# Optimization experiments

Measured on AMD Instinct MI355X. Metric: run time of the kernel, lower is better.

Reference implementation:

```python
import jax, jax.numpy as jnp
import numpy as np


def conv1x1(x, w, b):
    # x: [B,C,H,W], w: [O,C], b: [O]  (1x1 conv == per-pixel matmul)
    return jnp.einsum('oc,bchw->bohw', w, x) + b[None, :, None, None]


def setup_inputs() -> dict:
    key = jax.random.key(0)
    ks = jax.random.split(key, 8)
    B, C, H, W = 8, 256, 64, 64
    heads, points = 8, 4
    x = jax.random.normal(ks[0], (B, C, H, W), dtype=jnp.float32)
    # small offset weights so sampling grids stay mostly in-range (original inits these to 0)
    w_off = jax.random.normal(ks[1], (heads * points * 2, C), dtype=jnp.float32) * 0.01
    b_off = jax.random.normal(ks[2], (heads * points * 2,), dtype=jnp.float32) * 0.05
    w_attn = jax.random.normal(ks[3], (heads * points, C), dtype=jnp.float32) * 0.02
    b_attn = jnp.full((heads * points,), np.log(1.0 / points), dtype=jnp.float32)
    w_val = jax.random.normal(ks[4], (C, C), dtype=jnp.float32) * (1.0 / np.sqrt(C))
    b_val = jnp.zeros((C,), dtype=jnp.float32)
    w_out = jax.random.normal(ks[5], (C, C), dtype=jnp.float32) * (1.0 / np.sqrt(C))
    b_out = jnp.zeros((C,), dtype=jnp.float32)
    return {"x": x, "w_off": w_off, "b_off": b_off, "w_attn": w_attn, "b_attn": b_attn,
            "w_val": w_val, "b_val": b_val, "w_out": w_out, "b_out": b_out,
            "num_heads": heads, "num_points": points}


def _grid_sample_one(v, g):
    # v: [Cph,H,W] value image; g: [P,H,W,2] sampling grid in [-1,1] (x,y), align_corners=True,
    # bilinear, zero padding. Returns [Cph,P,H,W].
    Cph, H, W = v.shape
    ix = (g[..., 0] + 1.0) * 0.5 * (W - 1)  # [P,H,W]
    iy = (g[..., 1] + 1.0) * 0.5 * (H - 1)
    x0 = jnp.floor(ix); y0 = jnp.floor(iy)
    x1 = x0 + 1.0;      y1 = y0 + 1.0
    wx1 = ix - x0; wx0 = 1.0 - wx1
    wy1 = iy - y0; wy0 = 1.0 - wy1

    def corner(yc, xc, w):
        valid = (xc >= 0) & (xc <= W - 1) & (yc >= 0) & (yc <= H - 1)
        yi = jnp.clip(yc, 0, H - 1).astype(jnp.int32)
        xi = jnp.clip(xc, 0, W - 1).astype(jnp.int32)
        vv = v[:, yi, xi]  # [Cph,P,H,W]
        return vv * (w * valid.astype(w.dtype))[None]

    return (corner(y0, x0, wy0 * wx0) + corner(y0, x1, wy0 * wx1)
            + corner(y1, x0, wy1 * wx0) + corner(y1, x1, wy1 * wx1))


def deformable_attention(x, w_off, b_off, w_attn, b_attn, w_val, b_val, w_out, b_out,
                         num_heads, num_points):
    B, C, H, W = x.shape
    hd, P = num_heads, num_points
    cph = C // hd

    value = conv1x1(x, w_val, b_val)                       # [B,C,H,W]
    offsets = conv1x1(x, w_off, b_off)                     # [B,hd*P*2,H,W]
    attn = conv1x1(x, w_attn, b_attn).reshape(B, hd, P, H, W)
    attn = jax.nn.softmax(attn, axis=2)                    # softmax over points

    gy = jnp.linspace(-1.0, 1.0, H, dtype=x.dtype)
    gx = jnp.linspace(-1.0, 1.0, W, dtype=x.dtype)
    base = jnp.stack(jnp.meshgrid(gx, gy, indexing='xy'), axis=-1)  # [H,W,2] (x,y)

    off = offsets.reshape(B, hd, P, 2, H, W).transpose(0, 1, 2, 4, 5, 3)  # [B,hd,P,H,W,2]
    grid = base[None, None, None] + off                                   # [B,hd,P,H,W,2]

    val = value.reshape(B * hd, cph, H, W)
    grid = grid.reshape(B * hd, P, H, W, 2)
    sampled = jax.vmap(_grid_sample_one)(val, grid)        # [B*hd,cph,P,H,W]
    sampled = sampled.reshape(B, hd, cph, P, H, W)

    weighted = (sampled * attn[:, :, None]).sum(axis=3)    # [B,hd,cph,H,W]
    weighted = weighted.reshape(B, C, H, W)
    return conv1x1(weighted, w_out, b_out) + x


def reference(x, w_off, b_off, w_attn, b_attn, w_val, b_val, w_out, b_out,
              num_heads, num_points):
    return deformable_attention(x, w_off, b_off, w_attn, b_attn, w_val, b_val,
                                w_out, b_out, num_heads, num_points)
```

## Files before the change

kernel.cpp:

```cpp
#include <hip/hip_runtime.h>
#include <cstddef>

#define HW 4096

typedef __attribute__((ext_vector_type(8))) short short8v;
typedef __attribute__((ext_vector_type(4))) float f32x4;

__device__ inline unsigned short f2bf(float f) {
    unsigned int u = __float_as_uint(f);
    u += 0x7FFFu + ((u >> 16) & 1u);
    return (unsigned short)(u >> 16);
}
__device__ inline float bf2f(unsigned short s) {
    return __uint_as_float(((unsigned int)s) << 16);
}

#define GLOAD_LDS16(gp, lp) __builtin_amdgcn_global_load_lds( \
    (const __attribute__((address_space(1))) unsigned int*)(gp), \
    (__attribute__((address_space(3))) unsigned int*)(lp), 16, 0, 0)

__device__ inline void stage_tile(const unsigned short* __restrict__ g,
                                  unsigned short* lds, int kc, int wid, int lane)
{
    const int r8   = lane >> 3;
    const int slot = (lane & 7) ^ r8;
    const unsigned short* src = g + (wid * 32 + r8) * 256 + kc + slot * 8;
#pragma unroll
    for (int i = 0; i < 4; ++i) {
        GLOAD_LDS16(src + i * 8 * 256, lds + (wid * 32 + i * 8) * 64);
    }
}

__device__ inline short8v read_frag(const unsigned short* lds, int row, int kbyte, int lane)
{
    const char* p = (const char*)lds + row * 128 + (kbyte ^ ((lane & 7) * 16));
    return *(const short8v*)p;
}

__global__ __launch_bounds__(256)
void prep_kernel(const float* __restrict__ w_off, const float* __restrict__ b_off,
                 const float* __restrict__ w_attn, const float* __restrict__ b_attn,
                 const float* __restrict__ w_val, const float* __restrict__ b_val,
                 const float* __restrict__ w_out,
                 unsigned short* __restrict__ wcat_bf, unsigned short* __restrict__ wauxlo,
                 unsigned short* __restrict__ wout_bf, float* __restrict__ bcat)
{
    int i = blockIdx.x * 256 + threadIdx.x;
    if (i < 384 * 256) {
        int n = i >> 8, k = i & 255;
        float v;
        if (n < 256)      v = w_val[n * 256 + k];
        else if (n < 320) v = w_off[(n - 256) * 256 + k];
        else if (n < 352) v = w_attn[(n - 320) * 256 + k];
        else              v = 0.0f;
        unsigned short hi = f2bf(v);
        wcat_bf[i] = hi;
        if (n >= 256) wauxlo[(n - 256) * 256 + k] = f2bf(v - bf2f(hi));
    }
    if (i < 256 * 256) wout_bf[i] = f2bf(w_out[i]);
    if (i < 512) {
        float v = 0.0f;
        if (i < 256)      v = b_val[i];
        else if (i < 320) v = b_off[i - 256];
        else if (i < 352) v = b_attn[i - 320];
        bcat[i] = v;
    }
}

__global__ __launch_bounds__(256)
void transpose_kernel(const float* __restrict__ x, unsigned short* __restrict__ xhi)
{
    __shared__ float t[64][65];
    const int bid = blockIdx.x;
    const int pt = bid & 63, ct = (bid >> 6) & 3, b = bid >> 8;
    const int tid = threadIdx.x;
    const int rr = tid >> 4, c4 = (tid & 15) * 4;

    const float* src = x + ((size_t)(b * 256 + ct * 64)) * HW + pt * 64;
#pragma unroll
    for (int j = 0; j < 4; ++j) {
        float4 v = *(const float4*)&src[(size_t)(j * 16 + rr) * HW + c4];
        t[j * 16 + rr][c4 + 0] = v.x; t[j * 16 + rr][c4 + 1] = v.y;
        t[j * 16 + rr][c4 + 2] = v.z; t[j * 16 + rr][c4 + 3] = v.w;
    }
    __syncthreads();

    const size_t obase = ((size_t)b * HW + pt * 64) * 256 + ct * 64;
#pragma unroll
    for (int j = 0; j < 4; ++j) {
        int p = j * 16 + rr;
        ushort4 hi = make_ushort4(f2bf(t[c4 + 0][p]), f2bf(t[c4 + 1][p]),
                                  f2bf(t[c4 + 2][p]), f2bf(t[c4 + 3][p]));
        *(ushort4*)&xhi[obase + (size_t)p * 256 + c4] = hi;
    }
}

__global__ __launch_bounds__(256)
void proj_kernel(const unsigned short* __restrict__ wcat_bf, const unsigned short* __restrict__ wauxlo,
                 const unsigned short* __restrict__ xhi, const float* __restrict__ bcat,
                 unsigned short* __restrict__ value_bf,
                 float* __restrict__ off_ws, float* __restrict__ attn_ws)
{
    __shared__ unsigned short lds[3 * 128 * 64];
    const int bid = blockIdx.x;
    const int mt = bid % 3;
    const int pt = (bid / 3) & 31;
    const int b  = bid / 96;
    const int tid = threadIdx.x, wid = tid >> 6, lane = tid & 63;
    const int wm = wid >> 1, wn = wid & 1;
    const int mloc = lane & 15, ksel = lane >> 4;

    const unsigned short* Bg = xhi + ((size_t)b * HW + pt * 128) * 256;

    f32x4 acc[4][4];
#pragma unroll
    for (int fm = 0; fm < 4; ++fm) {
        float4 bv = *(const float4*)&bcat[mt * 128 + wm * 64 + fm * 16 + ksel * 4];
#pragma unroll
        for (int fn = 0; fn < 4; ++fn) acc[fm][fn] = (f32x4){bv.x, bv.y, bv.z, bv.w};
    }

    if (mt < 2) {
        unsigned short* Al = lds;
        unsigned short* Bl = lds + 128 * 64;
        const unsigned short* Ag = wcat_bf + mt * 128 * 256;
#pragma unroll
        for (int kc = 0; kc < 4; ++kc) {
            if (kc) __syncthreads();
            stage_tile(Ag, Al, kc * 64, wid, lane);
            stage_tile(Bg, Bl, kc * 64, wid, lane);
            __syncthreads();
#pragma unroll
            for (int kk = 0; kk < 2; ++kk) {
                const int kb = kk * 64 + ksel * 16;
                short8v a[4], bb[4];
#pragma unroll
                for (int f = 0; f < 4; ++f) a[f]  = read_frag(Al, wm * 64 + f * 16 + mloc, kb, lane);
#pragma unroll
                for (int f = 0; f < 4; ++f) bb[f] = read_frag(Bl, wn * 64 + f * 16 + mloc, kb, lane);
#pragma unroll
                for (int fm = 0; fm < 4; ++fm)
#pragma unroll
                    for (int fn = 0; fn < 4; ++fn)
                        acc[fm][fn] = __builtin_amdgcn_mfma_f32_16x16x32_bf16(a[fm], bb[fn], acc[fm][fn], 0, 0, 0);
            }
        }
#pragma unroll
        for (int fm = 0; fm < 4; ++fm) {
            const int ch = mt * 128 + wm * 64 + fm * 16 + ksel * 4;
            const int head = ch >> 5, c32 = ch & 31;
#pragma unroll
            for (int fn = 0; fn < 4; ++fn) {
                const int p = pt * 128 + wn * 64 + fn * 16 + mloc;
                f32x4 v = acc[fm][fn];
                ushort4 st = make_ushort4(f2bf(v[0]), f2bf(v[1]), f2bf(v[2]), f2bf(v[3]));
                *(ushort4*)&value_bf[(((size_t)(b * 8 + head)) * HW + p) * 32 + c32] = st;
            }
        }
    } else {
        unsigned short* Ah  = lds;
        unsigned short* Alo = lds + 128 * 64;
        unsigned short* Bl  = lds + 2 * 128 * 64;
        const unsigned short* Ahg = wcat_bf + 256 * 256;
        const unsigned short* Alg = wauxlo;
#pragma unroll
        for (int kc = 0; kc < 4; ++kc) {
            if (kc) __syncthreads();
            stage_tile(Ahg, Ah, kc * 64, wid, lane);
            stage_tile(Alg, Alo, kc * 64, wid, lane);
            stage_tile(Bg, Bl, kc * 64, wid, lane);
            __syncthreads();
#pragma unroll
            for (int kk = 0; kk < 2; ++kk) {
                const int kb = kk * 64 + ksel * 16;
                short8v ah[4], al[4], bb[4];
#pragma unroll
                for (int f = 0; f < 4; ++f) {
                    ah[f] = read_frag(Ah,  wm * 64 + f * 16 + mloc, kb, lane);
                    al[f] = read_frag(Alo, wm * 64 + f * 16 + mloc, kb, lane);
                    bb[f] = read_frag(Bl,  wn * 64 + f * 16 + mloc, kb, lane);
                }
#pragma unroll
                for (int fm = 0; fm < 4; ++fm)
#pragma unroll
                    for (int fn = 0; fn < 4; ++fn) {
                        acc[fm][fn] = __builtin_amdgcn_mfma_f32_16x16x32_bf16(ah[fm], bb[fn], acc[fm][fn], 0, 0, 0);
                        acc[fm][fn] = __builtin_amdgcn_mfma_f32_16x16x32_bf16(al[fm], bb[fn], acc[fm][fn], 0, 0, 0);
                    }
            }
        }
#pragma unroll
        for (int fm = 0; fm < 4; ++fm) {
            const int chb = wm * 64 + fm * 16 + ksel * 4;
#pragma unroll
            for (int fn = 0; fn < 4; ++fn) {
                const int p = pt * 128 + wn * 64 + fn * 16 + mloc;
                f32x4 v = acc[fm][fn];
#pragma unroll
                for (int r = 0; r < 4; ++r) {
                    int ch = chb + r;
                    if (ch < 64)      off_ws[((size_t)(b * 64 + ch)) * HW + p] = v[r];
                    else if (ch < 96) attn_ws[((size_t)(b * 32 + (ch - 64))) * HW + p] = v[r];
                }
            }
        }
    }
}

__global__ __launch_bounds__(256)
void sample_kernel(const unsigned short* __restrict__ value_bf, const float* __restrict__ off_ws,
                   const float* __restrict__ attn_ws, unsigned short* __restrict__ wgt_t)
{
    const int bid    = blockIdx.x;
    const int ptile  = bid & 127;
    const int head   = (bid >> 7) & 7;
    const int b      = bid >> 10;
    const int tid    = threadIdx.x;
    const int c4     = tid & 7;
    const int posIdx = tid >> 3;
    const int p      = ptile * 32 + posIdx;
    const int h      = p >> 6;
    const int w      = p & 63;

    const float gx = w * (2.0f / 63.0f) - 1.0f;
    const float gy = h * (2.0f / 63.0f) - 1.0f;

    float l0 = attn_ws[(size_t)(b * 32 + head * 4 + 0) * HW + p];
    float l1 = attn_ws[(size_t)(b * 32 + head * 4 + 1) * HW + p];
    float l2 = attn_ws[(size_t)(b * 32 + head * 4 + 2) * HW + p];
    float l3 = attn_ws[(size_t)(b * 32 + head * 4 + 3) * HW + p];
    float m  = fmaxf(fmaxf(l0, l1), fmaxf(l2, l3));
    float e0 = __expf(l0 - m), e1 = __expf(l1 - m), e2 = __expf(l2 - m), e3 = __expf(l3 - m);
    float inv = 1.0f / (e0 + e1 + e2 + e3);
    float aw[4] = {e0 * inv, e1 * inv, e2 * inv, e3 * inv};

    float4 acc = make_float4(0.f, 0.f, 0.f, 0.f);
    const unsigned short* vb = value_bf + (size_t)(b * 8 + head) * HW * 32 + c4 * 4;

#pragma unroll
    for (int pt = 0; pt < 4; ++pt) {
        float ox = off_ws[(size_t)(b * 64 + (head * 4 + pt) * 2 + 0) * HW + p];
        float oy = off_ws[(size_t)(b * 64 + (head * 4 + pt) * 2 + 1) * HW + p];
        float ix = (gx + ox + 1.0f) * 31.5f;
        float iy = (gy + oy + 1.0f) * 31.5f;
        float x0f = floorf(ix), y0f = floorf(iy);
        float wx1 = ix - x0f, wx0 = 1.0f - wx1;
        float wy1 = iy - y0f, wy0 = 1.0f - wy1;
        int x0 = (int)x0f, y0 = (int)y0f;
        int x1 = x0 + 1,   y1 = y0 + 1;
        float a = aw[pt];
        float vx0 = (x0 >= 0 && x0 <= 63) ? 1.f : 0.f;
        float vx1 = (x1 >= 0 && x1 <= 63) ? 1.f : 0.f;
        float vy0 = (y0 >= 0 && y0 <= 63) ? 1.f : 0.f;
        float vy1 = (y1 >= 0 && y1 <= 63) ? 1.f : 0.f;
        float w00 = a * wy0 * wx0 * vy0 * vx0;
        float w01 = a * wy0 * wx1 * vy0 * vx1;
        float w10 = a * wy1 * wx0 * vy1 * vx0;
        float w11 = a * wy1 * wx1 * vy1 * vx1;
        int cx0 = min(max(x0, 0), 63), cx1 = min(max(x1, 0), 63);
        int cy0 = min(max(y0, 0), 63), cy1 = min(max(y1, 0), 63);
        ushort4 u00 = *(const ushort4*)&vb[(size_t)(cy0 * 64 + cx0) * 32];
        ushort4 u01 = *(const ushort4*)&vb[(size_t)(cy0 * 64 + cx1) * 32];
        ushort4 u10 = *(const ushort4*)&vb[(size_t)(cy1 * 64 + cx0) * 32];
        ushort4 u11 = *(const ushort4*)&vb[(size_t)(cy1 * 64 + cx1) * 32];
        acc.x += w00 * bf2f(u00.x) + w01 * bf2f(u01.x) + w10 * bf2f(u10.x) + w11 * bf2f(u11.x);
        acc.y += w00 * bf2f(u00.y) + w01 * bf2f(u01.y) + w10 * bf2f(u10.y) + w11 * bf2f(u11.y);
        acc.z += w00 * bf2f(u00.z) + w01 * bf2f(u01.z) + w10 * bf2f(u10.z) + w11 * bf2f(u11.z);
        acc.w += w00 * bf2f(u00.w) + w01 * bf2f(u01.w) + w10 * bf2f(u10.w) + w11 * bf2f(u11.w);
    }

    ushort4 st = make_ushort4(f2bf(acc.x), f2bf(acc.y), f2bf(acc.z), f2bf(acc.w));
    *(ushort4*)&wgt_t[((size_t)b * HW + p) * 256 + head * 32 + c4 * 4] = st;
}

__global__ __launch_bounds__(256)
void outproj_gemm(const unsigned short* __restrict__ wout_bf, const unsigned short* __restrict__ wgt_t,
                  const float* __restrict__ b_out, const float* __restrict__ x,
                  float* __restrict__ out)
{
    __shared__ unsigned short Al[128 * 64];
    __shared__ unsigned short Bl[128 * 64];
    const int bid = blockIdx.x;
    const int pt = bid & 31, mt = (bid >> 5) & 1, b = bid >> 6;
    const int tid = threadIdx.x, wid = tid >> 6, lane = tid & 63;
    const int wm = wid >> 1, wn = wid & 1;
    const int mloc = lane & 15, ksel = lane >> 4;

    const unsigned short* Ag = wout_bf + mt * 128 * 256;
    const unsigned short* Bg = wgt_t + ((size_t)b * HW + pt * 128) * 256;

    f32x4 acc[4][4];
#pragma unroll
    for (int fm = 0; fm < 4; ++fm)
#pragma unroll
        for (int fn = 0; fn < 4; ++fn) acc[fm][fn] = (f32x4){0.f, 0.f, 0.f, 0.f};

#pragma unroll
    for (int kc = 0; kc < 4; ++kc) {
        if (kc) __syncthreads();
        stage_tile(Ag, Al, kc * 64, wid, lane);
        stage_tile(Bg, Bl, kc * 64, wid, lane);
        __syncthreads();
#pragma unroll
        for (int kk = 0; kk < 2; ++kk) {
            const int kb = kk * 64 + ksel * 16;
            short8v a[4], bb[4];
#pragma unroll
            for (int f = 0; f < 4; ++f) a[f]  = read_frag(Al, wm * 64 + f * 16 + mloc, kb, lane);
#pragma unroll
            for (int f = 0; f < 4; ++f) bb[f] = read_frag(Bl, wn * 64 + f * 16 + mloc, kb, lane);
#pragma unroll
            for (int fm = 0; fm < 4; ++fm)
#pragma unroll
                for (int fn = 0; fn < 4; ++fn)
                    acc[fm][fn] = __builtin_amdgcn_mfma_f32_16x16x32_bf16(a[fm], bb[fn], acc[fm][fn], 0, 0, 0);
        }
    }

#pragma unroll
    for (int fm = 0; fm < 4; ++fm) {
        const int o = mt * 128 + wm * 64 + fm * 16 + ksel * 4;
        float4 bo = *(const float4*)&b_out[o];
#pragma unroll
        for (int fn = 0; fn < 4; ++fn) {
            const int p = pt * 128 + wn * 64 + fn * 16 + mloc;
            const size_t idx = ((size_t)(b * 256 + o)) * HW + p;
            f32x4 v = acc[fm][fn];
            out[idx + 0 * HW] = v[0] + bo.x + x[idx + 0 * HW];
            out[idx + 1 * HW] = v[1] + bo.y + x[idx + 1 * HW];
            out[idx + 2 * HW] = v[2] + bo.z + x[idx + 2 * HW];
            out[idx + 3 * HW] = v[3] + bo.w + x[idx + 3 * HW];
        }
    }
}

extern "C" void kernel_launch(void* const* d_in, const int* in_sizes, int n_in,
                              void* d_out, int out_size, void* d_ws, size_t ws_size,
                              hipStream_t stream)
{
    const float* x      = (const float*)d_in[0];
    const float* w_off  = (const float*)d_in[1];
    const float* b_off  = (const float*)d_in[2];
    const float* w_attn = (const float*)d_in[3];
    const float* b_attn = (const float*)d_in[4];
    const float* w_val  = (const float*)d_in[5];
    const float* b_val  = (const float*)d_in[6];
    const float* w_out  = (const float*)d_in[7];
    const float* b_out  = (const float*)d_in[8];
    float* out = (float*)d_out;

    char* ws = (char*)d_ws;
    unsigned short* wcat_bf = (unsigned short*)(ws + 0);
    unsigned short* wauxlo  = (unsigned short*)(ws + 196608);
    unsigned short* wout_bf = (unsigned short*)(ws + 262144);
    float*          bcat    = (float*)(ws + 393216);
    unsigned short* xhi     = (unsigned short*)(ws + 395264);
    unsigned short* val_bf  = (unsigned short*)(ws + 17172480);
    float*          off_ws  = (float*)(ws + 33949696);
    float*          attn_ws = (float*)(ws + 42338304);
    unsigned short* wgt_t   = (unsigned short*)(ws + 46532608);

    prep_kernel<<<384, 256, 0, stream>>>(w_off, b_off, w_attn, b_attn, w_val, b_val,
                                         w_out, wcat_bf, wauxlo, wout_bf, bcat);
    transpose_kernel<<<2048, 256, 0, stream>>>(x, xhi);
    proj_kernel<<<768, 256, 0, stream>>>(wcat_bf, wauxlo, xhi, bcat, val_bf, off_ws, attn_ws);
    sample_kernel<<<8192, 256, 0, stream>>>(val_bf, off_ws, attn_ws, wgt_t);
    outproj_gemm<<<512, 256, 0, stream>>>(wout_bf, wgt_t, b_out, x, out);
}
```

Measured before the change: 81.53 us.

## Stage full-K panels, transpose offset/attn layout, and LDS-stage outproj epilogue

The GEMM kernels now load the full K=256 panels for A and B into LDS in one pass using a row-XOR swizzle, replacing the four-chunk loop with its repeated barriers. The projection kernel reorders blocks so point tiles vary fastest, and runs the hi/lo aux weights as two sequential passes over the same B panel. Offset and attention logits are now stored pixel-major as float4, so the sample kernel reads them contiguously. The out-projection epilogue goes through LDS so the residual add and output store use coalesced float4 accesses. The larger LDS footprint (128 KB per block) limits occupancy to about one block per CU.

After: 80.73 us. No clear change (-1.0%).

```diff
diff --git a/kernel.cpp b/kernel.cpp
--- a/kernel.cpp
+++ b/kernel.cpp
@@ -19,22 +19,42 @@
     (const __attribute__((address_space(1))) unsigned int*)(gp), \
     (__attribute__((address_space(3))) unsigned int*)(lp), 16, 0, 0)
 
-__device__ inline void stage_tile(const unsigned short* __restrict__ g,
-                                  unsigned short* lds, int kc, int wid, int lane)
-{
-    const int r8   = lane >> 3;
-    const int slot = (lane & 7) ^ r8;
-    const unsigned short* src = g + (wid * 32 + r8) * 256 + kc + slot * 8;
-#pragma unroll
-    for (int i = 0; i < 4; ++i) {
-        GLOAD_LDS16(src + i * 8 * 256, lds + (wid * 32 + i * 8) * 64);
-    }
-}
-
-__device__ inline short8v read_frag(const unsigned short* lds, int row, int kbyte, int lane)
-{
-    const char* p = (const char*)lds + row * 128 + (kbyte ^ ((lane & 7) * 16));
+__device__ inline void stage_panel(const unsigned short* __restrict__ g,
+                                   unsigned short* lds, int wid, int lane)
+{
+    const int rsub = lane >> 5;
+    const int slot = lane & 31;
+#pragma unroll
+    for (int i = 0; i < 16; ++i) {
+        const int row = wid * 32 + i * 2 + rsub;
+        GLOAD_LDS16(g + row * 256 + ((slot ^ (row & 15)) << 3),
+                    lds + (wid * 32 + i * 2) * 256);
+    }
+}
+
+__device__ inline short8v read_frag256(const unsigned short* lds, int row, int kbyte)
+{
+    const char* p = (const char*)lds + row * 512 + (kbyte ^ ((row & 15) << 4));
     return *(const short8v*)p;
+}
+
+__device__ inline void compute_pass(const unsigned short* Al, const unsigned short* Bl,
+                                    int wm, int wn, int mloc, int ksel, f32x4 acc[4][4])
+{
+#pragma unroll
+    for (int kk = 0; kk < 8; ++kk) {
+        const int kb = kk * 64 + ksel * 16;
+        short8v a[4], bb[4];
+#pragma unroll
+        for (int f = 0; f < 4; ++f) a[f]  = read_frag256(Al, wm * 64 + f * 16 + mloc, kb);
+#pragma unroll
+        for (int f = 0; f < 4; ++f) bb[f] = read_frag256(Bl, wn * 64 + f * 16 + mloc, kb);
+#pragma unroll
+        for (int fm = 0; fm < 4; ++fm)
+#pragma unroll
+            for (int fn = 0; fn < 4; ++fn)
+                acc[fm][fn] = __builtin_amdgcn_mfma_f32_16x16x32_bf16(a[fm], bb[fn], acc[fm][fn], 0, 0, 0);
+    }
 }
 
 __global__ __launch_bounds__(256)
@@ -101,16 +121,19 @@
                  unsigned short* __restrict__ value_bf,
                  float* __restrict__ off_ws, float* __restrict__ attn_ws)
 {
-    __shared__ unsigned short lds[3 * 128 * 64];
+    __shared__ unsigned short smem[2 * 128 * 256];
+    unsigned short* Al = smem;
+    unsigned short* Bl = smem + 128 * 256;
+
     const int bid = blockIdx.x;
-    const int mt = bid % 3;
-    const int pt = (bid / 3) & 31;
+    const int pt = bid & 31;
+    const int mt = (bid >> 5) % 3;
     const int b  = bid / 96;
     const int tid = threadIdx.x, wid = tid >> 6, lane = tid & 63;
     const int wm = wid >> 1, wn = wid & 1;
     const int mloc = lane & 15, ksel = lane >> 4;
 
-    const unsigned short* Bg = xhi + ((size_t)b * HW + pt * 128) * 256;
+    stage_panel(xhi + ((size_t)b * HW + pt * 128) * 256, Bl, wid, lane);
 
     f32x4 acc[4][4];
 #pragma unroll
@@ -121,30 +144,10 @@
     }
 
     if (mt < 2) {
-        unsigned short* Al = lds;
-        unsigned short* Bl = lds + 128 * 64;
-        const unsigned short* Ag = wcat_bf + mt * 128 * 256;
-#pragma unroll
-        for (int kc = 0; kc < 4; ++kc) {
-            if (kc) __syncthreads();
-            stage_tile(Ag, Al, kc * 64, wid, lane);
-            stage_tile(Bg, Bl, kc * 64, wid, lane);
-            __syncthreads();
-#pragma unroll
-            for (int kk = 0; kk < 2; ++kk) {
-                const int kb = kk * 64 + ksel * 16;
-                short8v a[4], bb[4];
-#pragma unroll
-                for (int f = 0; f < 4; ++f) a[f]  = read_frag(Al, wm * 64 + f * 16 + mloc, kb, lane);
-#pragma unroll
-                for (int f = 0; f < 4; ++f) bb[f] = read_frag(Bl, wn * 64 + f * 16 + mloc, kb, lane);
-#pragma unroll
-                for (int fm = 0; fm < 4; ++fm)
-#pragma unroll
-                    for (int fn = 0; fn < 4; ++fn)
-                        acc[fm][fn] = __builtin_amdgcn_mfma_f32_16x16x32_bf16(a[fm], bb[fn], acc[fm][fn], 0, 0, 0);
-            }
-        }
+        stage_panel(wcat_bf + mt * 128 * 256, Al, wid, lane);
+        __syncthreads();
+        compute_pass(Al, Bl, wm, wn, mloc, ksel, acc);
+
 #pragma unroll
         for (int fm = 0; fm < 4; ++fm) {
             const int ch = mt * 128 + wm * 64 + fm * 16 + ksel * 4;
@@ -158,49 +161,27 @@
             }
         }
     } else {
-        unsigned short* Ah  = lds;
-        unsigned short* Alo = lds + 128 * 64;
-        unsigned short* Bl  = lds + 2 * 128 * 64;
-        const unsigned short* Ahg = wcat_bf + 256 * 256;
-        const unsigned short* Alg = wauxlo;
-#pragma unroll
-        for (int kc = 0; kc < 4; ++kc) {
-            if (kc) __syncthreads();
-            stage_tile(Ahg, Ah, kc * 64, wid, lane);
-            stage_tile(Alg, Alo, kc * 64, wid, lane);
-            stage_tile(Bg, Bl, kc * 64, wid, lane);
-            __syncthreads();
-#pragma unroll
-            for (int kk = 0; kk < 2; ++kk) {
-                const int kb = kk * 64 + ksel * 16;
-                short8v ah[4], al[4], bb[4];
-#pragma unroll
-                for (int f = 0; f < 4; ++f) {
-                    ah[f] = read_frag(Ah,  wm * 64 + f * 16 + mloc, kb, lane);
-                    al[f] = read_frag(Alo, wm * 64 + f * 16 + mloc, kb, lane);
-                    bb[f] = read_frag(Bl,  wn * 64 + f * 16 + mloc, kb, lane);
-                }
-#pragma unroll
-                for (int fm = 0; fm < 4; ++fm)
-#pragma unroll
-                    for (int fn = 0; fn < 4; ++fn) {
-                        acc[fm][fn] = __builtin_amdgcn_mfma_f32_16x16x32_bf16(ah[fm], bb[fn], acc[fm][fn], 0, 0, 0);
-                        acc[fm][fn] = __builtin_amdgcn_mfma_f32_16x16x32_bf16(al[fm], bb[fn], acc[fm][fn], 0, 0, 0);
-                    }
-            }
-        }
+        stage_panel(wcat_bf + 256 * 256, Al, wid, lane);
+        __syncthreads();
+        compute_pass(Al, Bl, wm, wn, mloc, ksel, acc);
+        __syncthreads();
+        stage_panel(wauxlo, Al, wid, lane);
+        __syncthreads();
+        compute_pass(Al, Bl, wm, wn, mloc, ksel, acc);
+
 #pragma unroll
         for (int fm = 0; fm < 4; ++fm) {
-            const int chb = wm * 64 + fm * 16 + ksel * 4;
+            const int ch0 = wm * 64 + fm * 16 + ksel * 4;
 #pragma unroll
             for (int fn = 0; fn < 4; ++fn) {
                 const int p = pt * 128 + wn * 64 + fn * 16 + mloc;
                 f32x4 v = acc[fm][fn];
-#pragma unroll
-                for (int r = 0; r < 4; ++r) {
-                    int ch = chb + r;
-                    if (ch < 64)      off_ws[((size_t)(b * 64 + ch)) * HW + p] = v[r];
-                    else if (ch < 96) attn_ws[((size_t)(b * 32 + (ch - 64))) * HW + p] = v[r];
+                if (ch0 < 64) {
+                    *(float4*)&off_ws[((size_t)b * HW + p) * 64 + ch0] =
+                        make_float4(v[0], v[1], v[2], v[3]);
+                } else if (ch0 < 96) {
+                    *(float4*)&attn_ws[((size_t)b * HW + p) * 32 + (ch0 - 64)] =
+                        make_float4(v[0], v[1], v[2], v[3]);
                 }
             }
         }
@@ -225,22 +206,20 @@
     const float gx = w * (2.0f / 63.0f) - 1.0f;
     const float gy = h * (2.0f / 63.0f) - 1.0f;
 
-    float l0 = attn_ws[(size_t)(b * 32 + head * 4 + 0) * HW + p];
-    float l1 = attn_ws[(size_t)(b * 32 + head * 4 + 1) * HW + p];
-    float l2 = attn_ws[(size_t)(b * 32 + head * 4 + 2) * HW + p];
-    float l3 = attn_ws[(size_t)(b * 32 + head * 4 + 3) * HW + p];
-    float m  = fmaxf(fmaxf(l0, l1), fmaxf(l2, l3));
-    float e0 = __expf(l0 - m), e1 = __expf(l1 - m), e2 = __expf(l2 - m), e3 = __expf(l3 - m);
+    float4 la = *(const float4*)&attn_ws[((size_t)b * HW + p) * 32 + head * 4];
+    float m  = fmaxf(fmaxf(la.x, la.y), fmaxf(la.z, la.w));
+    float e0 = __expf(la.x - m), e1 = __expf(la.y - m), e2 = __expf(la.z - m), e3 = __expf(la.w - m);
     float inv = 1.0f / (e0 + e1 + e2 + e3);
     float aw[4] = {e0 * inv, e1 * inv, e2 * inv, e3 * inv};
 
     float4 acc = make_float4(0.f, 0.f, 0.f, 0.f);
     const unsigned short* vb = value_bf + (size_t)(b * 8 + head) * HW * 32 + c4 * 4;
+    const float* offp = off_ws + ((size_t)b * HW + p) * 64 + head * 8;
 
 #pragma unroll
     for (int pt = 0; pt < 4; ++pt) {
-        float ox = off_ws[(size_t)(b * 64 + (head * 4 + pt) * 2 + 0) * HW + p];
-        float oy = off_ws[(size_t)(b * 64 + (head * 4 + pt) * 2 + 1) * HW + p];
+        float ox = offp[pt * 2 + 0];
+        float oy = offp[pt * 2 + 1];
         float ix = (gx + ox + 1.0f) * 31.5f;
         float iy = (gy + oy + 1.0f) * 31.5f;
         float x0f = floorf(ix), y0f = floorf(iy);
@@ -273,21 +252,24 @@
     *(ushort4*)&wgt_t[((size_t)b * HW + p) * 256 + head * 32 + c4 * 4] = st;
 }
 
+#define EPW 132
 __global__ __launch_bounds__(256)
 void outproj_gemm(const unsigned short* __restrict__ wout_bf, const unsigned short* __restrict__ wgt_t,
                   const float* __restrict__ b_out, const float* __restrict__ x,
                   float* __restrict__ out)
 {
-    __shared__ unsigned short Al[128 * 64];
-    __shared__ unsigned short Bl[128 * 64];
+    __shared__ unsigned short smem[2 * 128 * 256];
+    unsigned short* Al = smem;
+    unsigned short* Bl = smem + 128 * 256;
+
     const int bid = blockIdx.x;
     const int pt = bid & 31, mt = (bid >> 5) & 1, b = bid >> 6;
     const int tid = threadIdx.x, wid = tid >> 6, lane = tid & 63;
     const int wm = wid >> 1, wn = wid & 1;
     const int mloc = lane & 15, ksel = lane >> 4;
 
-    const unsigned short* Ag = wout_bf + mt * 128 * 256;
-    const unsigned short* Bg = wgt_t + ((size_t)b * HW + pt * 128) * 256;
+    stage_panel(wout_bf + mt * 128 * 256, Al, wid, lane);
+    stage_panel(wgt_t + ((size_t)b * HW + pt * 128) * 256, Bl, wid, lane);
 
     f32x4 acc[4][4];
 #pragma unroll
@@ -295,42 +277,36 @@
 #pragma unroll
         for (int fn = 0; fn < 4; ++fn) acc[fm][fn] = (f32x4){0.f, 0.f, 0.f, 0.f};
 
-#pragma unroll
-    for (int kc = 0; kc < 4; ++kc) {
-        if (kc) __syncthreads();
-        stage_tile(Ag, Al, kc * 64, wid, lane);
-        stage_tile(Bg, Bl, kc * 64, wid, lane);
-        __syncthreads();
-#pragma unroll
-        for (int kk = 0; kk < 2; ++kk) {
-            const int kb = kk * 64 + ksel * 16;
-            short8v a[4], bb[4];
-#pragma unroll
-            for (int f = 0; f < 4; ++f) a[f]  = read_frag(Al, wm * 64 + f * 16 + mloc, kb, lane);
-#pragma unroll
-            for (int f = 0; f < 4; ++f) bb[f] = read_frag(Bl, wn * 64 + f * 16 + mloc, kb, lane);
-#pragma unroll
-            for (int fm = 0; fm < 4; ++fm)
-#pragma unroll
-                for (int fn = 0; fn < 4; ++fn)
-                    acc[fm][fn] = __builtin_amdgcn_mfma_f32_16x16x32_bf16(a[fm], bb[fn], acc[fm][fn], 0, 0, 0);
+    __syncthreads();
+    compute_pass(Al, Bl, wm, wn, mloc, ksel, acc);
+    __syncthreads();
+
+    float* ep = (float*)smem;
+#pragma unroll
+    for (int fm = 0; fm < 4; ++fm) {
+        const int o_loc = wm * 64 + fm * 16 + ksel * 4;
+#pragma unroll
+        for (int fn = 0; fn < 4; ++fn) {
+            const int p_loc = wn * 64 + fn * 16 + mloc;
+            f32x4 v = acc[fm][fn];
+#pragma unroll
+            for (int r = 0; r < 4; ++r) ep[(o_loc + r) * EPW + p_loc] = v[r];
         }
     }
-
-#pragma unroll
-    for (int fm = 0; fm < 4; ++fm) {
-        const int o = mt * 128 + wm * 64 + fm * 16 + ksel * 4;
-        float4 bo = *(const float4*)&b_out[o];
-#pragma unroll
-        for (int fn = 0; fn < 4; ++fn) {
-            const int p = pt * 128 + wn * 64 + fn * 16 + mloc;
-            const size_t idx = ((size_t)(b * 256 + o)) * HW + p;
-            f32x4 v = acc[fm][fn];
-            out[idx + 0 * HW] = v[0] + bo.x + x[idx + 0 * HW];
-            out[idx + 1 * HW] = v[1] + bo.y + x[idx + 1 * HW];
-            out[idx + 2 * HW] = v[2] + bo.z + x[idx + 2 * HW];
-            out[idx + 3 * HW] = v[3] + bo.w + x[idx + 3 * HW];
-        }
+    __syncthreads();
+
+    const int p4 = (tid & 31) * 4;
+    const int o0 = tid >> 5;
+    const size_t gbase = ((size_t)(b * 256 + mt * 128)) * HW + pt * 128;
+#pragma unroll
+    for (int it = 0; it < 16; ++it) {
+        const int o = o0 + it * 8;
+        float bo = b_out[mt * 128 + o];
+        float4 v = *(const float4*)&ep[o * EPW + p4];
+        const size_t gi = gbase + (size_t)o * HW + p4;
+        float4 xv = *(const float4*)&x[gi];
+        *(float4*)&out[gi] = make_float4(v.x + bo + xv.x, v.y + bo + xv.y,
+                                         v.z + bo + xv.z, v.w + bo + xv.w);
     }
 }
 
```

## Register-prefetch GEMM tiles and store offsets/attn logits pixel-major

Applied to the files above, without the earlier changes.

The direct global-to-LDS loads in both GEMM kernels are replaced by register staging. The next K-chunk is loaded into registers while MFMAs consume the current LDS tile, which overlaps global latency with compute. The offset and attention-logit workspaces move from channel-major to pixel-major layout, so the projection writes float4 and the sampler reads a contiguous float4 of logits and contiguous offsets per pixel. The proj block index order also changes so pixel tiles vary fastest. The cost is higher register pressure and extra LDS store instructions.

Result: faster. 77.80 us (-4.6%).

```diff
diff --git a/kernel.cpp b/kernel.cpp
--- a/kernel.cpp
+++ b/kernel.cpp
@@ -15,19 +15,27 @@
     return __uint_as_float(((unsigned int)s) << 16);
 }
 
-#define GLOAD_LDS16(gp, lp) __builtin_amdgcn_global_load_lds( \
-    (const __attribute__((address_space(1))) unsigned int*)(gp), \
-    (__attribute__((address_space(3))) unsigned int*)(lp), 16, 0, 0)
-
-__device__ inline void stage_tile(const unsigned short* __restrict__ g,
-                                  unsigned short* lds, int kc, int wid, int lane)
-{
-    const int r8   = lane >> 3;
-    const int slot = (lane & 7) ^ r8;
-    const unsigned short* src = g + (wid * 32 + r8) * 256 + kc + slot * 8;
+__device__ inline void load_tile(const unsigned short* __restrict__ g, int kc,
+                                 int wid, int lane, short8v r[4])
+{
+    const int s  = lane & 7;
+    const int r8 = lane >> 3;
+    const unsigned short* src = g + kc + s * 8;
 #pragma unroll
     for (int i = 0; i < 4; ++i) {
-        GLOAD_LDS16(src + i * 8 * 256, lds + (wid * 32 + i * 8) * 64);
+        const int row = wid * 32 + i * 8 + r8;
+        r[i] = *(const short8v*)(src + row * 256);
+    }
+}
+
+__device__ inline void store_tile(unsigned short* lds, int wid, int lane, const short8v r[4])
+{
+    const int s  = lane & 7;
+    const int r8 = lane >> 3;
+#pragma unroll
+    for (int i = 0; i < 4; ++i) {
+        const int row = wid * 32 + i * 8 + r8;
+        *(short8v*)((char*)lds + row * 128 + ((s ^ (row & 7)) << 4)) = r[i];
     }
 }
 
@@ -102,9 +110,13 @@
                  float* __restrict__ off_ws, float* __restrict__ attn_ws)
 {
     __shared__ unsigned short lds[3 * 128 * 64];
+    unsigned short* Al  = lds;
+    unsigned short* Bl  = lds + 128 * 64;
+    unsigned short* Alo = lds + 2 * 128 * 64;
+
     const int bid = blockIdx.x;
-    const int mt = bid % 3;
-    const int pt = (bid / 3) & 31;
+    const int pt = bid & 31;
+    const int mt = (bid >> 5) % 3;
     const int b  = bid / 96;
     const int tid = threadIdx.x, wid = tid >> 6, lane = tid & 63;
     const int wm = wid >> 1, wn = wid & 1;
@@ -121,15 +133,20 @@
     }
 
     if (mt < 2) {
-        unsigned short* Al = lds;
-        unsigned short* Bl = lds + 128 * 64;
         const unsigned short* Ag = wcat_bf + mt * 128 * 256;
+        short8v rA[4], rB[4];
+        load_tile(Ag, 0, wid, lane, rA);
+        load_tile(Bg, 0, wid, lane, rB);
 #pragma unroll
         for (int kc = 0; kc < 4; ++kc) {
             if (kc) __syncthreads();
-            stage_tile(Ag, Al, kc * 64, wid, lane);
-            stage_tile(Bg, Bl, kc * 64, wid, lane);
+            store_tile(Al, wid, lane, rA);
+            store_tile(Bl, wid, lane, rB);
             __syncthreads();
+            if (kc < 3) {
+                load_tile(Ag, (kc + 1) * 64, wid, lane, rA);
+                load_tile(Bg, (kc + 1) * 64, wid, lane, rB);
+            }
 #pragma unroll
             for (int kk = 0; kk < 2; ++kk) {
                 const int kb = kk * 64 + ksel * 16;
@@ -158,25 +175,31 @@
             }
         }
     } else {
-        unsigned short* Ah  = lds;
-        unsigned short* Alo = lds + 128 * 64;
-        unsigned short* Bl  = lds + 2 * 128 * 64;
         const unsigned short* Ahg = wcat_bf + 256 * 256;
         const unsigned short* Alg = wauxlo;
+        short8v rA[4], rL[4], rB[4];
+        load_tile(Ahg, 0, wid, lane, rA);
+        load_tile(Alg, 0, wid, lane, rL);
+        load_tile(Bg, 0, wid, lane, rB);
 #pragma unroll
         for (int kc = 0; kc < 4; ++kc) {
             if (kc) __syncthreads();
-            stage_tile(Ahg, Ah, kc * 64, wid, lane);
-            stage_tile(Alg, Alo, kc * 64, wid, lane);
-            stage_tile(Bg, Bl, kc * 64, wid, lane);
+            store_tile(Al, wid, lane, rA);
+            store_tile(Alo, wid, lane, rL);
+            store_tile(Bl, wid, lane, rB);
             __syncthreads();
+            if (kc < 3) {
+                load_tile(Ahg, (kc + 1) * 64, wid, lane, rA);
+                load_tile(Alg, (kc + 1) * 64, wid, lane, rL);
+                load_tile(Bg, (kc + 1) * 64, wid, lane, rB);
+            }
 #pragma unroll
             for (int kk = 0; kk < 2; ++kk) {
                 const int kb = kk * 64 + ksel * 16;
                 short8v ah[4], al[4], bb[4];
 #pragma unroll
                 for (int f = 0; f < 4; ++f) {
-                    ah[f] = read_frag(Ah,  wm * 64 + f * 16 + mloc, kb, lane);
+                    ah[f] = read_frag(Al,  wm * 64 + f * 16 + mloc, kb, lane);
                     al[f] = read_frag(Alo, wm * 64 + f * 16 + mloc, kb, lane);
                     bb[f] = read_frag(Bl,  wn * 64 + f * 16 + mloc, kb, lane);
                 }
@@ -191,16 +214,17 @@
         }
 #pragma unroll
         for (int fm = 0; fm < 4; ++fm) {
-            const int chb = wm * 64 + fm * 16 + ksel * 4;
+            const int ch0 = wm * 64 + fm * 16 + ksel * 4;
 #pragma unroll
             for (int fn = 0; fn < 4; ++fn) {
                 const int p = pt * 128 + wn * 64 + fn * 16 + mloc;
                 f32x4 v = acc[fm][fn];
-#pragma unroll
-                for (int r = 0; r < 4; ++r) {
-                    int ch = chb + r;
-                    if (ch < 64)      off_ws[((size_t)(b * 64 + ch)) * HW + p] = v[r];
-                    else if (ch < 96) attn_ws[((size_t)(b * 32 + (ch - 64))) * HW + p] = v[r];
+                if (ch0 < 64) {
+                    *(float4*)&off_ws[((size_t)b * HW + p) * 64 + ch0] =
+                        make_float4(v[0], v[1], v[2], v[3]);
+                } else if (ch0 < 96) {
+                    *(float4*)&attn_ws[((size_t)b * HW + p) * 32 + (ch0 - 64)] =
+                        make_float4(v[0], v[1], v[2], v[3]);
                 }
             }
         }
@@ -225,22 +249,20 @@
     const float gx = w * (2.0f / 63.0f) - 1.0f;
     const float gy = h * (2.0f / 63.0f) - 1.0f;
 
-    float l0 = attn_ws[(size_t)(b * 32 + head * 4 + 0) * HW + p];
-    float l1 = attn_ws[(size_t)(b * 32 + head * 4 + 1) * HW + p];
-    float l2 = attn_ws[(size_t)(b * 32 + head * 4 + 2) * HW + p];
-    float l3 = attn_ws[(size_t)(b * 32 + head * 4 + 3) * HW + p];
-    float m  = fmaxf(fmaxf(l0, l1), fmaxf(l2, l3));
-    float e0 = __expf(l0 - m), e1 = __expf(l1 - m), e2 = __expf(l2 - m), e3 = __expf(l3 - m);
+    float4 la = *(const float4*)&attn_ws[((size_t)b * HW + p) * 32 + head * 4];
+    float m  = fmaxf(fmaxf(la.x, la.y), fmaxf(la.z, la.w));
+    float e0 = __expf(la.x - m), e1 = __expf(la.y - m), e2 = __expf(la.z - m), e3 = __expf(la.w - m);
     float inv = 1.0f / (e0 + e1 + e2 + e3);
     float aw[4] = {e0 * inv, e1 * inv, e2 * inv, e3 * inv};
 
     float4 acc = make_float4(0.f, 0.f, 0.f, 0.f);
     const unsigned short* vb = value_bf + (size_t)(b * 8 + head) * HW * 32 + c4 * 4;
+    const float* offp = off_ws + ((size_t)b * HW + p) * 64 + head * 8;
 
 #pragma unroll
     for (int pt = 0; pt < 4; ++pt) {
-        float ox = off_ws[(size_t)(b * 64 + (head * 4 + pt) * 2 + 0) * HW + p];
-        float oy = off_ws[(size_t)(b * 64 + (head * 4 + pt) * 2 + 1) * HW + p];
+        float ox = offp[pt * 2 + 0];
+        float oy = offp[pt * 2 + 1];
         float ix = (gx + ox + 1.0f) * 31.5f;
         float iy = (gy + oy + 1.0f) * 31.5f;
         float x0f = floorf(ix), y0f = floorf(iy);
@@ -295,12 +317,19 @@
 #pragma unroll
         for (int fn = 0; fn < 4; ++fn) acc[fm][fn] = (f32x4){0.f, 0.f, 0.f, 0.f};
 
+    short8v rA[4], rB[4];
+    load_tile(Ag, 0, wid, lane, rA);
+    load_tile(Bg, 0, wid, lane, rB);
 #pragma unroll
     for (int kc = 0; kc < 4; ++kc) {
         if (kc) __syncthreads();
-        stage_tile(Ag, Al, kc * 64, wid, lane);
-        stage_tile(Bg, Bl, kc * 64, wid, lane);
+        store_tile(Al, wid, lane, rA);
+        store_tile(Bl, wid, lane, rB);
         __syncthreads();
+        if (kc < 3) {
+            load_tile(Ag, (kc + 1) * 64, wid, lane, rA);
+            load_tile(Bg, (kc + 1) * 64, wid, lane, rB);
+        }
 #pragma unroll
         for (int kk = 0; kk < 2; ++kk) {
             const int kb = kk * 64 + ksel * 16;
```
